# Kernel tuning notes

Hardware: AMD Instinct MI355X
Metric: run time of the kernel (lower is better)

The kernel has to match this reference:

```python
import jax, jax.numpy as jnp
import numpy as np

N_NODES = 100000
N_EDGES = 1600000
DIMS = [100, 200, 128, 128]
EPS = 1e-5


def setup_inputs() -> dict:
    key = jax.random.key(0)
    ks = jax.random.split(key, 32)
    inp = {
        "x": jax.random.normal(ks[0], (N_NODES, DIMS[0]), dtype=jnp.float32),
        "edge_row": jnp.sort(jax.random.randint(ks[1], (N_EDGES,), 0, N_NODES, dtype=jnp.int32)),
        "edge_col": jax.random.randint(ks[2], (N_EDGES,), 0, N_NODES, dtype=jnp.int32),
        "edge_val": jax.random.uniform(ks[3], (N_EDGES,), dtype=jnp.float32),
    }
    # GCwithself layer params: neighbor-agg linear W,b and self linear Ws,bs
    ki = 4
    for i in range(3):
        fi, fo = DIMS[i], DIMS[i + 1]
        s = 1.0 / np.sqrt(fi)
        inp[f"gc{i}_W"] = jax.random.uniform(ks[ki], (fi, fo), minval=-s, maxval=s); ki += 1
        inp[f"gc{i}_b"] = jnp.zeros((fo,), jnp.float32)
        inp[f"gc{i}_Ws"] = jax.random.uniform(ks[ki], (fi, fo), minval=-s, maxval=s); ki += 1
        inp[f"gc{i}_bs"] = jnp.zeros((fo,), jnp.float32)
    s = 1.0 / np.sqrt(128)
    inp["fc1_W"] = jax.random.uniform(ks[ki], (128, 128), minval=-s, maxval=s); ki += 1
    inp["fc1_b"] = jnp.zeros((128,), jnp.float32)
    inp["fc2a_W"] = jax.random.uniform(ks[ki], (128, 256), minval=-s, maxval=s); ki += 1
    inp["fc2a_b"] = jnp.zeros((256,), jnp.float32)
    inp["bn_g"] = jnp.ones((256,), jnp.float32)
    inp["bn_b"] = jnp.zeros((256,), jnp.float32)
    s2 = 1.0 / np.sqrt(256)
    inp["fc2b_W"] = jax.random.uniform(ks[ki], (256, 18), minval=-s2, maxval=s2); ki += 1
    inp["fc2b_b"] = jnp.zeros((18,), jnp.float32)
    return inp


def _gc_layer(x, row, col, val, W, b, Ws, bs):
    # spmm: (adj @ x) via gather + segment-sum, then linear + self-linear + ReLU
    agg = jax.ops.segment_sum(val[:, None] * x[col], row, num_segments=N_NODES)
    return jax.nn.relu(agg @ W + b + x @ Ws + bs)


def _batchnorm(h, g, b):
    mu = jnp.mean(h, axis=0)
    var = jnp.var(h, axis=0)
    return (h - mu) * jax.lax.rsqrt(var + EPS) * g + b


def reference(x, edge_row, edge_col, edge_val,
              gc0_W, gc0_b, gc0_Ws, gc0_bs,
              gc1_W, gc1_b, gc1_Ws, gc1_bs,
              gc2_W, gc2_b, gc2_Ws, gc2_bs,
              fc1_W, fc1_b, fc2a_W, fc2a_b, bn_g, bn_b, fc2b_W, fc2b_b):
    h = _gc_layer(x, edge_row, edge_col, edge_val, gc0_W, gc0_b, gc0_Ws, gc0_bs)
    h = _gc_layer(h, edge_row, edge_col, edge_val, gc1_W, gc1_b, gc1_Ws, gc1_bs)
    h = _gc_layer(h, edge_row, edge_col, edge_val, gc2_W, gc2_b, gc2_Ws, gc2_bs)
    h = jax.nn.relu(h @ fc1_W + fc1_b)
    h = _batchnorm(h @ fc2a_W + fc2a_b, bn_g, bn_b)
    h = jax.nn.relu(h)
    return h @ fc2b_W + fc2b_b
```

## Files before the change

kernel.cpp:

```cpp
#include <hip/hip_runtime.h>

#define N_NODES 100000
#define N_EDGES 1600000

typedef __attribute__((ext_vector_type(8))) short bf16x8;
typedef __attribute__((ext_vector_type(4))) float f32x4;

__device__ __forceinline__ unsigned short f2bf(float f) {
    unsigned u = __float_as_uint(f);
    u = (u + 0x7FFFu + ((u >> 16) & 1u)) >> 16;
    return (unsigned short)u;
}
__device__ __forceinline__ float bf2f(unsigned short h) {
    return __uint_as_float(((unsigned)h) << 16);
}
__device__ __forceinline__ float bflo(unsigned w) { return __uint_as_float(w << 16); }
__device__ __forceinline__ float bfhi(unsigned w) { return __uint_as_float(w & 0xFFFF0000u); }

__device__ __forceinline__ bf16x8 ld_frag(const unsigned short* p) {
    return *(const bf16x8*)p;
}

__global__ void build_row_ptr(const int* __restrict__ row, int* __restrict__ rp) {
    int n = blockIdx.x * blockDim.x + threadIdx.x;
    if (n > N_NODES) return;
    int lo = 0, hi = N_EDGES;
    while (lo < hi) {
        int mid = (lo + hi) >> 1;
        if (row[mid] < n) lo = mid + 1; else hi = mid;
    }
    rp[n] = lo;
}

__global__ __launch_bounds__(256) void conv_x(const float* __restrict__ x,
                                              unsigned short* __restrict__ xb) {
    const int total = N_NODES * 104;
    for (int i = blockIdx.x * 256 + threadIdx.x; i < total; i += gridDim.x * 256) {
        int r = i / 104, c = i - r * 104;
        xb[i] = (c < 100) ? f2bf(x[(size_t)r * 100 + c]) : (unsigned short)0;
    }
}

__global__ __launch_bounds__(256) void prep_all(
    const float* __restrict__ gc0W, const float* __restrict__ gc0Ws,
    const float* __restrict__ gc1W, const float* __restrict__ gc1Ws,
    const float* __restrict__ gc2W, const float* __restrict__ gc2Ws,
    const float* __restrict__ f1W,  const float* __restrict__ f2aW,
    const float* __restrict__ f2bW,
    const float* __restrict__ gc0b, const float* __restrict__ gc0bs,
    const float* __restrict__ gc2b, const float* __restrict__ gc2bs,
    const float* __restrict__ gc1b, const float* __restrict__ gc1bs,
    unsigned short* __restrict__ Bt0, unsigned short* __restrict__ Bt1,
    unsigned short* __restrict__ Bt2, unsigned short* __restrict__ Btf1,
    unsigned short* __restrict__ Btf2a, unsigned short* __restrict__ Btf2b,
    float* __restrict__ bias0, float* __restrict__ bias2, float* __restrict__ bias1)
{
    int i = blockIdx.x * 256 + threadIdx.x;
    if (i < 44800) {
        int n = i / 224, k = i - n * 224; float v = 0.f;
        if (k < 104) { if (k < 100) v = gc0W[(size_t)k * 200 + n]; }
        else { int kr = k - 104; if (kr < 100) v = gc0Ws[(size_t)kr * 200 + n]; }
        Bt0[i] = f2bf(v); return;
    }
    i -= 44800;
    if (i < 57344) {
        int n = i / 224, k = i - n * 224; float v = 0.f;
        if (k < 200) v = (n < 128) ? gc1W[(size_t)k * 128 + n] : gc1Ws[(size_t)k * 128 + (n - 128)];
        Bt1[i] = f2bf(v); return;
    }
    i -= 57344;
    if (i < 32768) {
        int n = i / 256, k = i - n * 256; float v;
        if (k < 128) v = gc2W[(size_t)k * 128 + n];
        else         v = gc2Ws[(size_t)(k - 128) * 128 + n];
        Bt2[i] = f2bf(v); return;
    }
    i -= 32768;
    if (i < 16384) { int n = i >> 7, k = i & 127; Btf1[i] = f2bf(f1W[(size_t)k * 128 + n]); return; }
    i -= 16384;
    if (i < 32768) { int n = i >> 7, k = i & 127; Btf2a[i] = f2bf(f2aW[(size_t)k * 256 + n]); return; }
    i -= 32768;
    if (i < 4608) { int n = i >> 8, k = i & 255; Btf2b[i] = f2bf(f2bW[(size_t)k * 18 + n]); return; }
    i -= 4608;
    if (i < 200) { bias0[i] = gc0b[i] + gc0bs[i]; return; }
    i -= 200;
    if (i < 128) { bias2[i] = gc2b[i] + gc2bs[i]; return; }
    i -= 128;
    if (i < 128) { bias1[i] = gc1b[i] + gc1bs[i]; return; }
}

template<int FUSE>
__global__ __launch_bounds__(256) void spmm_v4(
    const unsigned short* __restrict__ xin, int ldin, int F,
    const int* __restrict__ rp, const int* __restrict__ col,
    const float* __restrict__ val, const float* __restrict__ b01,
    unsigned short* __restrict__ outp, int ldout)
{
    const int node = blockIdx.x * 16 + (threadIdx.x >> 4);
    const int l16 = threadIdx.x & 15;
    const int f8 = l16 * 8;
    const bool act = f8 < F;
    const int e0 = rp[node], e1 = rp[node + 1];
    const unsigned short* xf = xin + f8;

    float a[8];
#pragma unroll
    for (int k = 0; k < 8; k++) a[k] = 0.f;

    for (int e = e0; e < e1; e += 4) {
        int   cj[4]; float vj[4];
#pragma unroll
        for (int j = 0; j < 4; j++) {
            int ej = e + j;
            bool m = ej < e1;
            int es = m ? ej : e0;
            cj[j] = col[es];
            float vv = val[es];
            vj[j] = m ? vv : 0.f;
        }
        if (act) {
#pragma unroll
            for (int j = 0; j < 4; j++) {
                uint4 u = *(const uint4*)(xf + (size_t)cj[j] * ldin);
                float v = vj[j];
                a[0] += v * bflo(u.x); a[1] += v * bfhi(u.x);
                a[2] += v * bflo(u.y); a[3] += v * bfhi(u.y);
                a[4] += v * bflo(u.z); a[5] += v * bfhi(u.z);
                a[6] += v * bflo(u.w); a[7] += v * bfhi(u.w);
            }
        }
    }

    if (act) {
        if (FUSE) {
            uint4 uz = *(const uint4*)(xin + (size_t)node * ldin + 128 + f8);
            float z[8] = {bflo(uz.x), bfhi(uz.x), bflo(uz.y), bfhi(uz.y),
                          bflo(uz.z), bfhi(uz.z), bflo(uz.w), bfhi(uz.w)};
#pragma unroll
            for (int k = 0; k < 8; k++)
                a[k] = fmaxf(a[k] + z[k] + b01[f8 + k], 0.f);
        }
        uint4 pk;
        pk.x = ((unsigned)f2bf(a[1]) << 16) | (unsigned)f2bf(a[0]);
        pk.y = ((unsigned)f2bf(a[3]) << 16) | (unsigned)f2bf(a[2]);
        pk.z = ((unsigned)f2bf(a[5]) << 16) | (unsigned)f2bf(a[4]);
        pk.w = ((unsigned)f2bf(a[7]) << 16) | (unsigned)f2bf(a[6]);
        *(uint4*)(outp + (size_t)node * ldout + f8) = pk;
    }
}

__global__ __launch_bounds__(256) void gemm_head(
    const unsigned short* __restrict__ agg0, const unsigned short* __restrict__ xb,
    const unsigned short* __restrict__ Bt0, const float* __restrict__ bias0,
    const unsigned short* __restrict__ Bt1,
    unsigned short* __restrict__ yz, int M)
{
    __shared__ __align__(16) unsigned short H[64][264];

    const int tid = threadIdx.x;
    const int rowBase = blockIdx.x * 64;
    const int wave = tid >> 6, lane = tid & 63;
    const int cb = wave * 64;
    const int lrow = lane & 15, lq = lane >> 4;
    const int kq = lq * 8;

    {
        f32x4 acc[4][4] = {};
        bf16x8 afb[2][4], bfb[2][4];
        {
            int k0 = kq;
#pragma unroll
            for (int m = 0; m < 4; ++m) {
                int gr = rowBase + 16 * m + lrow;
                bf16x8 t = {};
                if (gr < M && k0 < 208)
                    t = (k0 < 104) ? ld_frag(agg0 + (size_t)gr * 104 + k0)
                                   : ld_frag(xb   + (size_t)gr * 104 + (k0 - 104));
                afb[0][m] = t;
            }
#pragma unroll
            for (int n = 0; n < 4; ++n) {
                int nr = cb + 16 * n + lrow;
                bf16x8 t = {};
                if (nr < 200) t = ld_frag(Bt0 + (size_t)nr * 224 + k0);
                bfb[0][n] = t;
            }
        }
#pragma unroll
        for (int ki = 0; ki < 7; ++ki) {
            const int cur = ki & 1;
            if (ki < 6) {
                const int nxt = cur ^ 1;
                int k0 = 32 * (ki + 1) + kq;
#pragma unroll
                for (int m = 0; m < 4; ++m) {
                    int gr = rowBase + 16 * m + lrow;
                    bf16x8 t = {};
                    if (gr < M && k0 < 208)
                        t = (k0 < 104) ? ld_frag(agg0 + (size_t)gr * 104 + k0)
                                       : ld_frag(xb   + (size_t)gr * 104 + (k0 - 104));
                    afb[nxt][m] = t;
                }
#pragma unroll
                for (int n = 0; n < 4; ++n) {
                    int nr = cb + 16 * n + lrow;
                    bf16x8 t = {};
                    if (nr < 200) t = ld_frag(Bt0 + (size_t)nr * 224 + k0);
                    bfb[nxt][n] = t;
                }
            }
#pragma unroll
            for (int m = 0; m < 4; ++m)
#pragma unroll
                for (int n = 0; n < 4; ++n)
                    acc[m][n] = __builtin_amdgcn_mfma_f32_16x16x32_bf16(afb[cur][m], bfb[cur][n], acc[m][n], 0, 0, 0);
        }
#pragma unroll
        for (int n = 0; n < 4; ++n) {
            int colg = cb + 16 * n + lrow;
            if (colg >= 224) continue;
            float bb = (colg < 200) ? bias0[colg] : 0.f;
#pragma unroll
            for (int m = 0; m < 4; ++m)
#pragma unroll
                for (int r = 0; r < 4; ++r) {
                    int rowl = 16 * m + lq * 4 + r;
                    H[rowl][colg] = f2bf(fmaxf(acc[m][n][r] + bb, 0.f));
                }
        }
    }
    __syncthreads();

    {
        f32x4 acc[4][4] = {};
        bf16x8 bfb[2][4];
#pragma unroll
        for (int n = 0; n < 4; ++n)
            bfb[0][n] = ld_frag(Bt1 + (size_t)(cb + 16 * n + lrow) * 224 + kq);
#pragma unroll
        for (int ki = 0; ki < 7; ++ki) {
            const int cur = ki & 1;
            if (ki < 6) {
                int k0 = 32 * (ki + 1) + kq;
#pragma unroll
                for (int n = 0; n < 4; ++n)
                    bfb[cur ^ 1][n] = ld_frag(Bt1 + (size_t)(cb + 16 * n + lrow) * 224 + k0);
            }
            int k0 = 32 * ki + kq;
            bf16x8 af[4];
#pragma unroll
            for (int m = 0; m < 4; ++m) af[m] = *(const bf16x8*)&H[16 * m + lrow][k0];
#pragma unroll
            for (int m = 0; m < 4; ++m)
#pragma unroll
                for (int n = 0; n < 4; ++n)
                    acc[m][n] = __builtin_amdgcn_mfma_f32_16x16x32_bf16(af[m], bfb[cur][n], acc[m][n], 0, 0, 0);
        }
        __syncthreads();
#pragma unroll
        for (int n = 0; n < 4; ++n) {
            int colg = cb + 16 * n + lrow;
#pragma unroll
            for (int m = 0; m < 4; ++m)
#pragma unroll
                for (int r = 0; r < 4; ++r) {
                    int rowl = 16 * m + lq * 4 + r;
                    H[rowl][colg] = f2bf(acc[m][n][r]);
                }
        }
    }
    __syncthreads();
#pragma unroll
    for (int i = 0; i < 8; ++i) {
        int c = tid + 256 * i;
        int row = c >> 5;
        int ch  = c & 31;
        int rowg = rowBase + row;
        if (rowg < M)
            *(uint4*)(yz + (size_t)rowg * 256 + ch * 8) = *(const uint4*)&H[row][ch * 8];
    }
}

__global__ __launch_bounds__(256) void gemm_tail(
    const unsigned short* __restrict__ agg2, const unsigned short* __restrict__ h1,
    const unsigned short* __restrict__ Bt2, const float* __restrict__ bias2,
    const unsigned short* __restrict__ Btf1, const float* __restrict__ fc1b,
    const unsigned short* __restrict__ Btf2a, const float* __restrict__ fc2ab,
    unsigned short* __restrict__ h4, float* __restrict__ stats, int M)
{
    __shared__ __align__(16) unsigned short H[64][264];

    const int tid = threadIdx.x;
    const int rowBase = blockIdx.x * 64;
    const int wave = tid >> 6, lane = tid & 63;
    const int lrow = lane & 15, lq = lane >> 4;
    const int kq = lq * 8;

    {
        const int cb = wave * 32;
        f32x4 acc[4][2] = {};
        bf16x8 afb[2][4], bfb[2][2];
        {
            int k0 = kq;
#pragma unroll
            for (int m = 0; m < 4; ++m) {
                int gr = rowBase + 16 * m + lrow;
                bf16x8 t = {};
                if (gr < M) t = ld_frag(agg2 + (size_t)gr * 128 + k0);
                afb[0][m] = t;
            }
#pragma unroll
            for (int n = 0; n < 2; ++n)
                bfb[0][n] = ld_frag(Bt2 + (size_t)(cb + 16 * n + lrow) * 256 + k0);
        }
#pragma unroll
        for (int ki = 0; ki < 8; ++ki) {
            const int cur = ki & 1;
            if (ki < 7) {
                const int nxt = cur ^ 1;
                const int kin = ki + 1;
                int k0 = 32 * kin + kq;
                const unsigned short* Asrc = (kin < 4) ? agg2 : h1;
                int krel = (kin < 4) ? k0 : k0 - 128;
#pragma unroll
                for (int m = 0; m < 4; ++m) {
                    int gr = rowBase + 16 * m + lrow;
                    bf16x8 t = {};
                    if (gr < M) t = ld_frag(Asrc + (size_t)gr * 128 + krel);
                    afb[nxt][m] = t;
                }
#pragma unroll
                for (int n = 0; n < 2; ++n)
                    bfb[nxt][n] = ld_frag(Bt2 + (size_t)(cb + 16 * n + lrow) * 256 + k0);
            }
#pragma unroll
            for (int m = 0; m < 4; ++m)
#pragma unroll
                for (int n = 0; n < 2; ++n)
                    acc[m][n] = __builtin_amdgcn_mfma_f32_16x16x32_bf16(afb[cur][m], bfb[cur][n], acc[m][n], 0, 0, 0);
        }
#pragma unroll
        for (int n = 0; n < 2; ++n) {
            int colg = cb + 16 * n + lrow;
            float bb = bias2[colg];
#pragma unroll
            for (int m = 0; m < 4; ++m)
#pragma unroll
                for (int r = 0; r < 4; ++r) {
                    int rowl = 16 * m + lq * 4 + r;
                    H[rowl][colg] = f2bf(fmaxf(acc[m][n][r] + bb, 0.f));
                }
        }
    }
    __syncthreads();

    {
        const int cb = wave * 32;
        f32x4 acc[4][2] = {};
        bf16x8 bfb[2][2];
#pragma unroll
        for (int n = 0; n < 2; ++n)
            bfb[0][n] = ld_frag(Btf1 + (size_t)(cb + 16 * n + lrow) * 128 + kq);
#pragma unroll
        for (int ki = 0; ki < 4; ++ki) {
            const int cur = ki & 1;
            if (ki < 3) {
                int k0 = 32 * (ki + 1) + kq;
#pragma unroll
                for (int n = 0; n < 2; ++n)
                    bfb[cur ^ 1][n] = ld_frag(Btf1 + (size_t)(cb + 16 * n + lrow) * 128 + k0);
            }
            int k0 = 32 * ki + kq;
            bf16x8 af[4];
#pragma unroll
            for (int m = 0; m < 4; ++m) af[m] = *(const bf16x8*)&H[16 * m + lrow][k0];
#pragma unroll
            for (int m = 0; m < 4; ++m)
#pragma unroll
                for (int n = 0; n < 2; ++n)
                    acc[m][n] = __builtin_amdgcn_mfma_f32_16x16x32_bf16(af[m], bfb[cur][n], acc[m][n], 0, 0, 0);
        }
        __syncthreads();
#pragma unroll
        for (int n = 0; n < 2; ++n) {
            int colg = cb + 16 * n + lrow;
            float bb = fc1b[colg];
#pragma unroll
            for (int m = 0; m < 4; ++m)
#pragma unroll
                for (int r = 0; r < 4; ++r) {
                    int rowl = 16 * m + lq * 4 + r;
                    H[rowl][colg] = f2bf(fmaxf(acc[m][n][r] + bb, 0.f));
                }
        }
    }
    __syncthreads();

    {
        const int cb = wave * 64;
        f32x4 acc[4][4] = {};
        bf16x8 bfb[2][4];
#pragma unroll
        for (int n = 0; n < 4; ++n)
            bfb[0][n] = ld_frag(Btf2a + (size_t)(cb + 16 * n + lrow) * 128 + kq);
#pragma unroll
        for (int ki = 0; ki < 4; ++ki) {
            const int cur = ki & 1;
            if (ki < 3) {
                int k0 = 32 * (ki + 1) + kq;
#pragma unroll
                for (int n = 0; n < 4; ++n)
                    bfb[cur ^ 1][n] = ld_frag(Btf2a + (size_t)(cb + 16 * n + lrow) * 128 + k0);
            }
            int k0 = 32 * ki + kq;
            bf16x8 af[4];
#pragma unroll
            for (int m = 0; m < 4; ++m) af[m] = *(const bf16x8*)&H[16 * m + lrow][k0];
#pragma unroll
            for (int m = 0; m < 4; ++m)
#pragma unroll
                for (int n = 0; n < 4; ++n)
                    acc[m][n] = __builtin_amdgcn_mfma_f32_16x16x32_bf16(af[m], bfb[cur][n], acc[m][n], 0, 0, 0);
        }
        __syncthreads();

#pragma unroll
        for (int n = 0; n < 4; ++n) {
            int colg = cb + 16 * n + lrow;
            float bb = fc2ab[colg];
            float s = 0.f, s2 = 0.f;
#pragma unroll
            for (int m = 0; m < 4; ++m)
#pragma unroll
                for (int r = 0; r < 4; ++r) {
                    int rowl = 16 * m + lq * 4 + r;
                    float v = acc[m][n][r] + bb;
                    H[rowl][colg] = f2bf(v);
                    if (rowBase + rowl < M) { s += v; s2 += v * v; }
                }
            s  += __shfl_xor(s, 16);  s  += __shfl_xor(s, 32);
            s2 += __shfl_xor(s2, 16); s2 += __shfl_xor(s2, 32);
            if (lq == 0) {
                atomicAdd(&stats[colg], s);
                atomicAdd(&stats[256 + colg], s2);
            }
        }
        __syncthreads();
#pragma unroll
        for (int i = 0; i < 8; ++i) {
            int c = tid + 256 * i;
            int row = c >> 5;
            int ch  = c & 31;
            int rowg = rowBase + row;
            if (rowg < M)
                *(uint4*)(h4 + (size_t)rowg * 256 + ch * 8) = *(const uint4*)&H[row][ch * 8];
        }
    }
}

__global__ void bn_finalize(float* __restrict__ stats,
                            const float* __restrict__ g,
                            const float* __restrict__ b) {
    int t = threadIdx.x;
    const float invN = 1.f / (float)N_NODES;
    float mu = stats[t] * invN;
    float var = stats[256 + t] * invN - mu * mu;
    float sc = g[t] * rsqrtf(var + 1e-5f);
    stats[512 + t] = sc;
    stats[768 + t] = b[t] - mu * sc;
}

__global__ __launch_bounds__(256) void fc2b_kernel(
    const unsigned short* __restrict__ h4, const unsigned short* __restrict__ Btf2b,
    const float* __restrict__ bias, const float* __restrict__ stats,
    float* __restrict__ out, int M)
{
    const int tid = threadIdx.x;
    const int wave = tid >> 6, lane = tid & 63;
    const int lrow = lane & 15, lq = lane >> 4;
    const int kq = lq * 8;
    const int rowBase = blockIdx.x * 128 + wave * 32;

    f32x4 acc[2][2] = {};
    uint4 ub[2][2];
    bf16x8 bfb[2][2];
#pragma unroll
    for (int m = 0; m < 2; ++m) {
        int gr = rowBase + 16 * m + lrow;
        uint4 u = make_uint4(0, 0, 0, 0);
        if (gr < M) u = *(const uint4*)(h4 + (size_t)gr * 256 + kq);
        ub[0][m] = u;
    }
#pragma unroll
    for (int n = 0; n < 2; ++n) {
        int nr = 16 * n + lrow;
        bf16x8 t = {};
        if (nr < 18) t = ld_frag(Btf2b + (size_t)nr * 256 + kq);
        bfb[0][n] = t;
    }
#pragma unroll
    for (int ki = 0; ki < 8; ++ki) {
        const int cur = ki & 1;
        if (ki < 7) {
            const int nxt = cur ^ 1;
            int k0 = 32 * (ki + 1) + kq;
#pragma unroll
            for (int m = 0; m < 2; ++m) {
                int gr = rowBase + 16 * m + lrow;
                uint4 u = make_uint4(0, 0, 0, 0);
                if (gr < M) u = *(const uint4*)(h4 + (size_t)gr * 256 + k0);
                ub[nxt][m] = u;
            }
#pragma unroll
            for (int n = 0; n < 2; ++n) {
                int nr = 16 * n + lrow;
                bf16x8 t = {};
                if (nr < 18) t = ld_frag(Btf2b + (size_t)nr * 256 + k0);
                bfb[nxt][n] = t;
            }
        }
        int k0 = 32 * ki + kq;
        const float* sc = stats + 512 + k0;
        const float* sh = stats + 768 + k0;
        bf16x8 af[2];
#pragma unroll
        for (int m = 0; m < 2; ++m) {
            unsigned w[4] = {ub[cur][m].x, ub[cur][m].y, ub[cur][m].z, ub[cur][m].w};
#pragma unroll
            for (int j = 0; j < 4; j++) {
                float lo = fmaxf(bflo(w[j]) * sc[2 * j] + sh[2 * j], 0.f);
                float hi = fmaxf(bfhi(w[j]) * sc[2 * j + 1] + sh[2 * j + 1], 0.f);
                w[j] = ((unsigned)f2bf(hi) << 16) | (unsigned)f2bf(lo);
            }
            uint4 packed = make_uint4(w[0], w[1], w[2], w[3]);
            af[m] = *(const bf16x8*)&packed;
        }
#pragma unroll
        for (int m = 0; m < 2; ++m)
#pragma unroll
            for (int n = 0; n < 2; ++n)
                acc[m][n] = __builtin_amdgcn_mfma_f32_16x16x32_bf16(af[m], bfb[cur][n], acc[m][n], 0, 0, 0);
    }
#pragma unroll
    for (int n = 0; n < 2; ++n) {
        int colg = 16 * n + lrow;
        if (colg >= 18) continue;
        float bb = bias[colg];
#pragma unroll
        for (int m = 0; m < 2; ++m)
#pragma unroll
            for (int r = 0; r < 4; ++r) {
                int rowg = rowBase + 16 * m + lq * 4 + r;
                if (rowg < M)
                    out[(size_t)rowg * 18 + colg] = acc[m][n][r] + bb;
            }
    }
}

extern "C" void kernel_launch(void* const* d_in, const int* in_sizes, int n_in,
                              void* d_out, int out_size, void* d_ws, size_t ws_size,
                              hipStream_t stream) {
    const float* x        = (const float*)d_in[0];
    const int*   edge_row = (const int*)  d_in[1];
    const int*   edge_col = (const int*)  d_in[2];
    const float* edge_val = (const float*)d_in[3];
    const float* gc0_W  = (const float*)d_in[4];
    const float* gc0_b  = (const float*)d_in[5];
    const float* gc0_Ws = (const float*)d_in[6];
    const float* gc0_bs = (const float*)d_in[7];
    const float* gc1_W  = (const float*)d_in[8];
    const float* gc1_b  = (const float*)d_in[9];
    const float* gc1_Ws = (const float*)d_in[10];
    const float* gc1_bs = (const float*)d_in[11];
    const float* gc2_W  = (const float*)d_in[12];
    const float* gc2_b  = (const float*)d_in[13];
    const float* gc2_Ws = (const float*)d_in[14];
    const float* gc2_bs = (const float*)d_in[15];
    const float* fc1_W  = (const float*)d_in[16];
    const float* fc1_b  = (const float*)d_in[17];
    const float* fc2a_W = (const float*)d_in[18];
    const float* fc2a_b = (const float*)d_in[19];
    const float* bn_g   = (const float*)d_in[20];
    const float* bn_b   = (const float*)d_in[21];
    const float* fc2b_W = (const float*)d_in[22];
    const float* fc2b_b = (const float*)d_in[23];
    float* out = (float*)d_out;

    char* ws = (char*)d_ws;
    int*   rowptr = (int*)ws;
    float* stats  = (float*)(ws + 512 * 1024);
    size_t o = 520 * 1024;
    unsigned short* Bt0   = (unsigned short*)(ws + o); o += 200 * 224 * 2;
    unsigned short* Bt1   = (unsigned short*)(ws + o); o += 256 * 224 * 2;
    unsigned short* Bt2   = (unsigned short*)(ws + o); o += 128 * 256 * 2;
    unsigned short* Btf1  = (unsigned short*)(ws + o); o += 128 * 128 * 2;
    unsigned short* Btf2a = (unsigned short*)(ws + o); o += 256 * 128 * 2;
    unsigned short* Btf2b = (unsigned short*)(ws + o); o += 18 * 256 * 2;
    float* bias0 = (float*)(ws + o); o += 200 * 4;
    float* bias2 = (float*)(ws + o); o += 128 * 4;
    float* bias1 = (float*)(ws + o); o += 128 * 4;
    const size_t SLOT = 52u * 1024 * 1024;
    char* S1 = ws + 1 * 1024 * 1024;
    char* S2 = S1 + SLOT;
    char* S3 = S2 + SLOT;

    unsigned short* xb   = (unsigned short*)S1;
    unsigned short* agg0 = (unsigned short*)S2;
    unsigned short* yz   = (unsigned short*)S3;
    unsigned short* h1   = (unsigned short*)S1;
    unsigned short* agg2 = (unsigned short*)S2;
    unsigned short* h4   = (unsigned short*)S3;

    build_row_ptr<<<392, 256, 0, stream>>>(edge_row, rowptr);
    conv_x<<<2048, 256, 0, stream>>>(x, xb);
    prep_all<<<(189128 + 255) / 256, 256, 0, stream>>>(
        gc0_W, gc0_Ws, gc1_W, gc1_Ws, gc2_W, gc2_Ws, fc1_W, fc2a_W, fc2b_W,
        gc0_b, gc0_bs, gc2_b, gc2_bs, gc1_b, gc1_bs,
        Bt0, Bt1, Bt2, Btf1, Btf2a, Btf2b, bias0, bias2, bias1);
    hipMemsetAsync(stats, 0, 512 * sizeof(float), stream);

    const int spmmGrid = N_NODES / 16;
    const int tile64 = (N_NODES + 63) / 64;

    spmm_v4<0><<<spmmGrid, 256, 0, stream>>>(xb, 104, 104, rowptr, edge_col, edge_val,
                                             nullptr, agg0, 104);
    gemm_head<<<tile64, 256, 0, stream>>>(agg0, xb, Bt0, bias0, Bt1, yz, N_NODES);
    spmm_v4<1><<<spmmGrid, 256, 0, stream>>>(yz, 256, 128, rowptr, edge_col, edge_val,
                                             bias1, h1, 128);
    spmm_v4<0><<<spmmGrid, 256, 0, stream>>>(h1, 128, 128, rowptr, edge_col, edge_val,
                                             nullptr, agg2, 128);
    gemm_tail<<<tile64, 256, 0, stream>>>(
        agg2, h1, Bt2, bias2, Btf1, fc1_b, Btf2a, fc2a_b, h4, stats, N_NODES);
    bn_finalize<<<1, 256, 0, stream>>>(stats, bn_g, bn_b);
    fc2b_kernel<<<(N_NODES + 127) / 128, 256, 0, stream>>>(
        h4, Btf2b, fc2b_b, stats, out, N_NODES);
}
```

Before: 516.2 us.

## Unroll SpMM gathers to eight edges and preload GEMM weight fragments

The SpMM kernel now gathers eight neighbor rows per iteration and issues all loads before the accumulates, so more memory requests are in flight per thread. The GEMM kernels (head, tail, fc2b) load all B-weight fragments for a K-chunk up front into registers and double-buffer only the A fragments. Compiler memory barriers are added to keep the load ordering. This raises register pressure, which could cut occupancy or cause spills.

Measured after the change: 525.0 us. Within noise of the previous version (+1.7%).

```diff
diff --git a/kernel.cpp b/kernel.cpp
--- a/kernel.cpp
+++ b/kernel.cpp
@@ -2,6 +2,8 @@
 
 #define N_NODES 100000
 #define N_EDGES 1600000
+
+#define MEMFENCE asm volatile("" ::: "memory")
 
 typedef __attribute__((ext_vector_type(8))) short bf16x8;
 typedef __attribute__((ext_vector_type(4))) float f32x4;
@@ -90,7 +92,7 @@
 }
 
 template<int FUSE>
-__global__ __launch_bounds__(256) void spmm_v4(
+__global__ __launch_bounds__(256) void spmm_v5(
     const unsigned short* __restrict__ xin, int ldin, int F,
     const int* __restrict__ rp, const int* __restrict__ col,
     const float* __restrict__ val, const float* __restrict__ b01,
@@ -107,10 +109,10 @@
 #pragma unroll
     for (int k = 0; k < 8; k++) a[k] = 0.f;
 
-    for (int e = e0; e < e1; e += 4) {
-        int   cj[4]; float vj[4];
-#pragma unroll
-        for (int j = 0; j < 4; j++) {
+    for (int e = e0; e < e1; e += 8) {
+        int   cj[8]; float vj[8];
+#pragma unroll
+        for (int j = 0; j < 8; j++) {
             int ej = e + j;
             bool m = ej < e1;
             int es = m ? ej : e0;
@@ -119,14 +121,17 @@
             vj[j] = m ? vv : 0.f;
         }
         if (act) {
-#pragma unroll
-            for (int j = 0; j < 4; j++) {
-                uint4 u = *(const uint4*)(xf + (size_t)cj[j] * ldin);
+            uint4 u[8];
+#pragma unroll
+            for (int j = 0; j < 8; j++)
+                u[j] = *(const uint4*)(xf + (size_t)cj[j] * ldin);
+#pragma unroll
+            for (int j = 0; j < 8; j++) {
                 float v = vj[j];
-                a[0] += v * bflo(u.x); a[1] += v * bfhi(u.x);
-                a[2] += v * bflo(u.y); a[3] += v * bfhi(u.y);
-                a[4] += v * bflo(u.z); a[5] += v * bfhi(u.z);
-                a[6] += v * bflo(u.w); a[7] += v * bfhi(u.w);
+                a[0] += v * bflo(u[j].x); a[1] += v * bfhi(u[j].x);
+                a[2] += v * bflo(u[j].y); a[3] += v * bfhi(u[j].y);
+                a[4] += v * bflo(u[j].z); a[5] += v * bfhi(u[j].z);
+                a[6] += v * bflo(u[j].w); a[7] += v * bfhi(u[j].w);
             }
         }
     }
@@ -166,54 +171,96 @@
 
     {
         f32x4 acc[4][4] = {};
-        bf16x8 afb[2][4], bfb[2][4];
         {
-            int k0 = kq;
+            bf16x8 Bf[4][4];
+#pragma unroll
+            for (int ki = 0; ki < 4; ++ki)
+#pragma unroll
+                for (int n = 0; n < 4; ++n) {
+                    int nr = cb + 16 * n + lrow;
+                    bf16x8 t = {};
+                    if (nr < 200) t = ld_frag(Bt0 + (size_t)nr * 224 + 32 * ki + kq);
+                    Bf[ki][n] = t;
+                }
+            MEMFENCE;
+            bf16x8 A2[2][4];
 #pragma unroll
             for (int m = 0; m < 4; ++m) {
                 int gr = rowBase + 16 * m + lrow;
                 bf16x8 t = {};
-                if (gr < M && k0 < 208)
-                    t = (k0 < 104) ? ld_frag(agg0 + (size_t)gr * 104 + k0)
-                                   : ld_frag(xb   + (size_t)gr * 104 + (k0 - 104));
-                afb[0][m] = t;
-            }
-#pragma unroll
-            for (int n = 0; n < 4; ++n) {
-                int nr = cb + 16 * n + lrow;
-                bf16x8 t = {};
-                if (nr < 200) t = ld_frag(Bt0 + (size_t)nr * 224 + k0);
-                bfb[0][n] = t;
-            }
-        }
-#pragma unroll
-        for (int ki = 0; ki < 7; ++ki) {
-            const int cur = ki & 1;
-            if (ki < 6) {
-                const int nxt = cur ^ 1;
-                int k0 = 32 * (ki + 1) + kq;
-#pragma unroll
-                for (int m = 0; m < 4; ++m) {
-                    int gr = rowBase + 16 * m + lrow;
-                    bf16x8 t = {};
-                    if (gr < M && k0 < 208)
-                        t = (k0 < 104) ? ld_frag(agg0 + (size_t)gr * 104 + k0)
-                                       : ld_frag(xb   + (size_t)gr * 104 + (k0 - 104));
-                    afb[nxt][m] = t;
-                }
+                if (gr < M)
+                    t = (kq < 104) ? ld_frag(agg0 + (size_t)gr * 104 + kq)
+                                   : ld_frag(xb   + (size_t)gr * 104 + (kq - 104));
+                A2[0][m] = t;
+            }
+            MEMFENCE;
+#pragma unroll
+            for (int ki = 0; ki < 4; ++ki) {
+                const int cur = ki & 1;
+                if (ki < 3) {
+                    int k0 = 32 * (ki + 1) + kq;
+#pragma unroll
+                    for (int m = 0; m < 4; ++m) {
+                        int gr = rowBase + 16 * m + lrow;
+                        bf16x8 t = {};
+                        if (gr < M)
+                            t = (k0 < 104) ? ld_frag(agg0 + (size_t)gr * 104 + k0)
+                                           : ld_frag(xb   + (size_t)gr * 104 + (k0 - 104));
+                        A2[cur ^ 1][m] = t;
+                    }
+                }
+                MEMFENCE;
+#pragma unroll
+                for (int m = 0; m < 4; ++m)
+#pragma unroll
+                    for (int n = 0; n < 4; ++n)
+                        acc[m][n] = __builtin_amdgcn_mfma_f32_16x16x32_bf16(A2[cur][m], Bf[ki][n], acc[m][n], 0, 0, 0);
+            }
+        }
+        {
+            bf16x8 Bf[3][4];
+#pragma unroll
+            for (int ki = 0; ki < 3; ++ki)
 #pragma unroll
                 for (int n = 0; n < 4; ++n) {
                     int nr = cb + 16 * n + lrow;
                     bf16x8 t = {};
-                    if (nr < 200) t = ld_frag(Bt0 + (size_t)nr * 224 + k0);
-                    bfb[nxt][n] = t;
-                }
-            }
-#pragma unroll
-            for (int m = 0; m < 4; ++m)
-#pragma unroll
-                for (int n = 0; n < 4; ++n)
-                    acc[m][n] = __builtin_amdgcn_mfma_f32_16x16x32_bf16(afb[cur][m], bfb[cur][n], acc[m][n], 0, 0, 0);
+                    if (nr < 200) t = ld_frag(Bt0 + (size_t)nr * 224 + 32 * (ki + 4) + kq);
+                    Bf[ki][n] = t;
+                }
+            MEMFENCE;
+            bf16x8 A2[2][4];
+#pragma unroll
+            for (int m = 0; m < 4; ++m) {
+                int gr = rowBase + 16 * m + lrow;
+                int k0 = 128 + kq;
+                bf16x8 t = {};
+                if (gr < M && k0 < 208)
+                    t = ld_frag(xb + (size_t)gr * 104 + (k0 - 104));
+                A2[0][m] = t;
+            }
+            MEMFENCE;
+#pragma unroll
+            for (int ki = 0; ki < 3; ++ki) {
+                const int cur = ki & 1;
+                if (ki < 2) {
+                    int k0 = 32 * (ki + 5) + kq;
+#pragma unroll
+                    for (int m = 0; m < 4; ++m) {
+                        int gr = rowBase + 16 * m + lrow;
+                        bf16x8 t = {};
+                        if (gr < M && k0 < 208)
+                            t = ld_frag(xb + (size_t)gr * 104 + (k0 - 104));
+                        A2[cur ^ 1][m] = t;
+                    }
+                }
+                MEMFENCE;
+#pragma unroll
+                for (int m = 0; m < 4; ++m)
+#pragma unroll
+                    for (int n = 0; n < 4; ++n)
+                        acc[m][n] = __builtin_amdgcn_mfma_f32_16x16x32_bf16(A2[cur][m], Bf[ki][n], acc[m][n], 0, 0, 0);
+            }
         }
 #pragma unroll
         for (int n = 0; n < 4; ++n) {
@@ -233,28 +280,45 @@
 
     {
         f32x4 acc[4][4] = {};
-        bf16x8 bfb[2][4];
-#pragma unroll
-        for (int n = 0; n < 4; ++n)
-            bfb[0][n] = ld_frag(Bt1 + (size_t)(cb + 16 * n + lrow) * 224 + kq);
-#pragma unroll
-        for (int ki = 0; ki < 7; ++ki) {
-            const int cur = ki & 1;
-            if (ki < 6) {
-                int k0 = 32 * (ki + 1) + kq;
+        {
+            bf16x8 Bf[4][4];
+#pragma unroll
+            for (int ki = 0; ki < 4; ++ki)
 #pragma unroll
                 for (int n = 0; n < 4; ++n)
-                    bfb[cur ^ 1][n] = ld_frag(Bt1 + (size_t)(cb + 16 * n + lrow) * 224 + k0);
-            }
-            int k0 = 32 * ki + kq;
-            bf16x8 af[4];
-#pragma unroll
-            for (int m = 0; m < 4; ++m) af[m] = *(const bf16x8*)&H[16 * m + lrow][k0];
-#pragma unroll
-            for (int m = 0; m < 4; ++m)
+                    Bf[ki][n] = ld_frag(Bt1 + (size_t)(cb + 16 * n + lrow) * 224 + 32 * ki + kq);
+            MEMFENCE;
+#pragma unroll
+            for (int ki = 0; ki < 4; ++ki) {
+                bf16x8 af[4];
+#pragma unroll
+                for (int m = 0; m < 4; ++m) af[m] = *(const bf16x8*)&H[16 * m + lrow][32 * ki + kq];
+#pragma unroll
+                for (int m = 0; m < 4; ++m)
+#pragma unroll
+                    for (int n = 0; n < 4; ++n)
+                        acc[m][n] = __builtin_amdgcn_mfma_f32_16x16x32_bf16(af[m], Bf[ki][n], acc[m][n], 0, 0, 0);
+            }
+        }
+        {
+            bf16x8 Bf[3][4];
+#pragma unroll
+            for (int ki = 0; ki < 3; ++ki)
 #pragma unroll
                 for (int n = 0; n < 4; ++n)
-                    acc[m][n] = __builtin_amdgcn_mfma_f32_16x16x32_bf16(af[m], bfb[cur][n], acc[m][n], 0, 0, 0);
+                    Bf[ki][n] = ld_frag(Bt1 + (size_t)(cb + 16 * n + lrow) * 224 + 32 * (ki + 4) + kq);
+            MEMFENCE;
+#pragma unroll
+            for (int ki = 0; ki < 3; ++ki) {
+                bf16x8 af[4];
+#pragma unroll
+                for (int m = 0; m < 4; ++m) af[m] = *(const bf16x8*)&H[16 * m + lrow][32 * (ki + 4) + kq];
+#pragma unroll
+                for (int m = 0; m < 4; ++m)
+#pragma unroll
+                    for (int n = 0; n < 4; ++n)
+                        acc[m][n] = __builtin_amdgcn_mfma_f32_16x16x32_bf16(af[m], Bf[ki][n], acc[m][n], 0, 0, 0);
+            }
         }
         __syncthreads();
 #pragma unroll
@@ -299,25 +363,26 @@
     {
         const int cb = wave * 32;
         f32x4 acc[4][2] = {};
-        bf16x8 afb[2][4], bfb[2][2];
-        {
-            int k0 = kq;
-#pragma unroll
-            for (int m = 0; m < 4; ++m) {
-                int gr = rowBase + 16 * m + lrow;
-                bf16x8 t = {};
-                if (gr < M) t = ld_frag(agg2 + (size_t)gr * 128 + k0);
-                afb[0][m] = t;
-            }
+        bf16x8 Bf[8][2];
+#pragma unroll
+        for (int ki = 0; ki < 8; ++ki)
 #pragma unroll
             for (int n = 0; n < 2; ++n)
-                bfb[0][n] = ld_frag(Bt2 + (size_t)(cb + 16 * n + lrow) * 256 + k0);
-        }
+                Bf[ki][n] = ld_frag(Bt2 + (size_t)(cb + 16 * n + lrow) * 256 + 32 * ki + kq);
+        MEMFENCE;
+        bf16x8 A2[2][4];
+#pragma unroll
+        for (int m = 0; m < 4; ++m) {
+            int gr = rowBase + 16 * m + lrow;
+            bf16x8 t = {};
+            if (gr < M) t = ld_frag(agg2 + (size_t)gr * 128 + kq);
+            A2[0][m] = t;
+        }
+        MEMFENCE;
 #pragma unroll
         for (int ki = 0; ki < 8; ++ki) {
             const int cur = ki & 1;
             if (ki < 7) {
-                const int nxt = cur ^ 1;
                 const int kin = ki + 1;
                 int k0 = 32 * kin + kq;
                 const unsigned short* Asrc = (kin < 4) ? agg2 : h1;
@@ -327,17 +392,15 @@
                     int gr = rowBase + 16 * m + lrow;
                     bf16x8 t = {};
                     if (gr < M) t = ld_frag(Asrc + (size_t)gr * 128 + krel);
-                    afb[nxt][m] = t;
-                }
+                    A2[cur ^ 1][m] = t;
+                }
+            }
+            MEMFENCE;
+#pragma unroll
+            for (int m = 0; m < 4; ++m)
 #pragma unroll
                 for (int n = 0; n < 2; ++n)
-                    bfb[nxt][n] = ld_frag(Bt2 + (size_t)(cb + 16 * n + lrow) * 256 + k0);
-            }
-#pragma unroll
-            for (int m = 0; m < 4; ++m)
-#pragma unroll
-                for (int n = 0; n < 2; ++n)
-                    acc[m][n] = __builtin_amdgcn_mfma_f32_16x16x32_bf16(afb[cur][m], bfb[cur][n], acc[m][n], 0, 0, 0);
+                    acc[m][n] = __builtin_amdgcn_mfma_f32_16x16x32_bf16(A2[cur][m], Bf[ki][n], acc[m][n], 0, 0, 0);
         }
 #pragma unroll
         for (int n = 0; n < 2; ++n) {
@@ -357,28 +420,23 @@
     {
         const int cb = wave * 32;
         f32x4 acc[4][2] = {};
-        bf16x8 bfb[2][2];
-#pragma unroll
-        for (int n = 0; n < 2; ++n)
-            bfb[0][n] = ld_frag(Btf1 + (size_t)(cb + 16 * n + lrow) * 128 + kq);
+        bf16x8 Bf[4][2];
+#pragma unroll
+        for (int ki = 0; ki < 4; ++ki)
+#pragma unroll
+            for (int n = 0; n < 2; ++n)
+                Bf[ki][n] = ld_frag(Btf1 + (size_t)(cb + 16 * n + lrow) * 128 + 32 * ki + kq);
+        MEMFENCE;
 #pragma unroll
         for (int ki = 0; ki < 4; ++ki) {
-            const int cur = ki & 1;
-            if (ki < 3) {
-                int k0 = 32 * (ki + 1) + kq;
+            bf16x8 af[4];
+#pragma unroll
+            for (int m = 0; m < 4; ++m) af[m] = *(const bf16x8*)&H[16 * m + lrow][32 * ki + kq];
+#pragma unroll
+            for (int m = 0; m < 4; ++m)
 #pragma unroll
                 for (int n = 0; n < 2; ++n)
-                    bfb[cur ^ 1][n] = ld_frag(Btf1 + (size_t)(cb + 16 * n + lrow) * 128 + k0);
-            }
-            int k0 = 32 * ki + kq;
-            bf16x8 af[4];
-#pragma unroll
-            for (int m = 0; m < 4; ++m) af[m] = *(const bf16x8*)&H[16 * m + lrow][k0];
-#pragma unroll
-            for (int m = 0; m < 4; ++m)
-#pragma unroll
-                for (int n = 0; n < 2; ++n)
-                    acc[m][n] = __builtin_amdgcn_mfma_f32_16x16x32_bf16(af[m], bfb[cur][n], acc[m][n], 0, 0, 0);
+                    acc[m][n] = __builtin_amdgcn_mfma_f32_16x16x32_bf16(af[m], Bf[ki][n], acc[m][n], 0, 0, 0);
         }
         __syncthreads();
 #pragma unroll
@@ -399,28 +457,23 @@
     {
         const int cb = wave * 64;
         f32x4 acc[4][4] = {};
-        bf16x8 bfb[2][4];
-#pragma unroll
-        for (int n = 0; n < 4; ++n)
-            bfb[0][n] = ld_frag(Btf2a + (size_t)(cb + 16 * n + lrow) * 128 + kq);
+        bf16x8 Bf[4][4];
+#pragma unroll
+        for (int ki = 0; ki < 4; ++ki)
+#pragma unroll
+            for (int n = 0; n < 4; ++n)
+                Bf[ki][n] = ld_frag(Btf2a + (size_t)(cb + 16 * n + lrow) * 128 + 32 * ki + kq);
+        MEMFENCE;
 #pragma unroll
         for (int ki = 0; ki < 4; ++ki) {
-            const int cur = ki & 1;
-            if (ki < 3) {
-                int k0 = 32 * (ki + 1) + kq;
+            bf16x8 af[4];
+#pragma unroll
+            for (int m = 0; m < 4; ++m) af[m] = *(const bf16x8*)&H[16 * m + lrow][32 * ki + kq];
+#pragma unroll
+            for (int m = 0; m < 4; ++m)
 #pragma unroll
                 for (int n = 0; n < 4; ++n)
-                    bfb[cur ^ 1][n] = ld_frag(Btf2a + (size_t)(cb + 16 * n + lrow) * 128 + k0);
-            }
-            int k0 = 32 * ki + kq;
-            bf16x8 af[4];
-#pragma unroll
-            for (int m = 0; m < 4; ++m) af[m] = *(const bf16x8*)&H[16 * m + lrow][k0];
-#pragma unroll
-            for (int m = 0; m < 4; ++m)
-#pragma unroll
-                for (int n = 0; n < 4; ++n)
-                    acc[m][n] = __builtin_amdgcn_mfma_f32_16x16x32_bf16(af[m], bfb[cur][n], acc[m][n], 0, 0, 0);
+                    acc[m][n] = __builtin_amdgcn_mfma_f32_16x16x32_bf16(af[m], Bf[ki][n], acc[m][n], 0, 0, 0);
         }
         __syncthreads();
 
@@ -482,8 +535,18 @@
     const int rowBase = blockIdx.x * 128 + wave * 32;
 
     f32x4 acc[2][2] = {};
+    bf16x8 Bf[8][2];
+#pragma unroll
+    for (int ki = 0; ki < 8; ++ki)
+#pragma unroll
+        for (int n = 0; n < 2; ++n) {
+            int nr = 16 * n + lrow;
+            bf16x8 t = {};
+            if (nr < 18) t = ld_frag(Btf2b + (size_t)nr * 256 + 32 * ki + kq);
+            Bf[ki][n] = t;
+        }
+    MEMFENCE;
     uint4 ub[2][2];
-    bf16x8 bfb[2][2];
 #pragma unroll
     for (int m = 0; m < 2; ++m) {
         int gr = rowBase + 16 * m + lrow;
@@ -491,34 +554,21 @@
         if (gr < M) u = *(const uint4*)(h4 + (size_t)gr * 256 + kq);
         ub[0][m] = u;
     }
-#pragma unroll
-    for (int n = 0; n < 2; ++n) {
-        int nr = 16 * n + lrow;
-        bf16x8 t = {};
-        if (nr < 18) t = ld_frag(Btf2b + (size_t)nr * 256 + kq);
-        bfb[0][n] = t;
-    }
+    MEMFENCE;
 #pragma unroll
     for (int ki = 0; ki < 8; ++ki) {
         const int cur = ki & 1;
         if (ki < 7) {
-            const int nxt = cur ^ 1;
             int k0 = 32 * (ki + 1) + kq;
 #pragma unroll
             for (int m = 0; m < 2; ++m) {
                 int gr = rowBase + 16 * m + lrow;
                 uint4 u = make_uint4(0, 0, 0, 0);
                 if (gr < M) u = *(const uint4*)(h4 + (size_t)gr * 256 + k0);
-                ub[nxt][m] = u;
-            }
-#pragma unroll
-            for (int n = 0; n < 2; ++n) {
-                int nr = 16 * n + lrow;
-                bf16x8 t = {};
-                if (nr < 18) t = ld_frag(Btf2b + (size_t)nr * 256 + k0);
-                bfb[nxt][n] = t;
-            }
-        }
+                ub[cur ^ 1][m] = u;
+            }
+        }
+        MEMFENCE;
         int k0 = 32 * ki + kq;
         const float* sc = stats + 512 + k0;
         const float* sh = stats + 768 + k0;
@@ -539,7 +589,7 @@
         for (int m = 0; m < 2; ++m)
 #pragma unroll
             for (int n = 0; n < 2; ++n)
-                acc[m][n] = __builtin_amdgcn_mfma_f32_16x16x32_bf16(af[m], bfb[cur][n], acc[m][n], 0, 0, 0);
+                acc[m][n] = __builtin_amdgcn_mfma_f32_16x16x32_bf16(af[m], Bf[ki][n], acc[m][n], 0, 0, 0);
     }
 #pragma unroll
     for (int n = 0; n < 2; ++n) {
@@ -622,12 +672,12 @@
     const int spmmGrid = N_NODES / 16;
     const int tile64 = (N_NODES + 63) / 64;
 
-    spmm_v4<0><<<spmmGrid, 256, 0, stream>>>(xb, 104, 104, rowptr, edge_col, edge_val,
+    spmm_v5<0><<<spmmGrid, 256, 0, stream>>>(xb, 104, 104, rowptr, edge_col, edge_val,
                                              nullptr, agg0, 104);
     gemm_head<<<tile64, 256, 0, stream>>>(agg0, xb, Bt0, bias0, Bt1, yz, N_NODES);
-    spmm_v4<1><<<spmmGrid, 256, 0, stream>>>(yz, 256, 128, rowptr, edge_col, edge_val,
+    spmm_v5<1><<<spmmGrid, 256, 0, stream>>>(yz, 256, 128, rowptr, edge_col, edge_val,
                                              bias1, h1, 128);
-    spmm_v4<0><<<spmmGrid, 256, 0, stream>>>(h1, 128, 128, rowptr, edge_col, edge_val,
+    spmm_v5<0><<<spmmGrid, 256, 0, stream>>>(h1, 128, 128, rowptr, edge_col, edge_val,
                                              nullptr, agg2, 128);
     gemm_tail<<<tile64, 256, 0, stream>>>(
         agg2, h1, Bt2, bias2, Btf1, fc1_b, Btf2a, fc2a_b, h4, stats, N_NODES);
```
